# Kernel tuning notes

Measured on AMD Instinct MI355X. Metric: run time of the kernel, lower is better.

The kernel has to match this reference:

```python
import jax, jax.numpy as jnp
import numpy as np

N, H, W = 128, 400, 400          # instances, feature canvas
MS = 28                          # mask_size = pooler_resolution*2
CT, CS = 80, 53                  # thing / stuff classes
STRIDE = 4                       # common_stride
HG, WG = 1600, 1600              # image-resolution gt panoptic
IGNORE = 255
LOSS_W = 1.0


def setup_inputs() -> dict:
    key = jax.random.key(0)
    ks = jax.random.split(key, 8)
    mask_logits = jax.random.normal(ks[0], (N, CT, MS, MS), jnp.float32)
    stuff_logit = jax.random.normal(ks[1], (CS, H, W), jnp.float32)
    thing_logit = jax.random.normal(ks[2], (CT, H, W), jnp.float32)
    # valid boxes in image pixel coords (x0,y0,x2,y2), width/height >= 16 px
    x0 = jax.random.uniform(ks[3], (N,), minval=0.0, maxval=1200.0)
    y0 = jax.random.uniform(ks[4], (N,), minval=0.0, maxval=1200.0)
    wh = jax.random.uniform(ks[5], (N, 2), minval=16.0, maxval=400.0)
    x2 = jnp.minimum(x0 + wh[:, 0], WG - 1.0)
    y2 = jnp.minimum(y0 + wh[:, 1], HG - 1.0)
    bbox = jnp.stack([x0, y0, x2, y2], axis=1).astype(jnp.float32)
    cls_idx = jax.random.randint(ks[6], (N,), 0, CT, dtype=jnp.int32)
    gt_panoptic = jax.random.randint(ks[7], (HG, WG), 0, CS + N, dtype=jnp.int32)
    return {"mask_logits": mask_logits, "stuff_logit": stuff_logit,
            "thing_logit": thing_logit, "bbox": bbox, "cls_idx": cls_idx,
            "gt_panoptic": gt_panoptic}


def _axis_sample(lo, size, grid, src_size):
    """Bilinear sampling coords along one axis (align_corners=False).
    lo: [N] box start (feat px, int); size: [N] box extent; grid: [G].
    Returns (idx0, idx1, frac) each [N, G]."""
    dst = grid[None, :].astype(jnp.float32) - lo[:, None].astype(jnp.float32)
    src = (dst + 0.5) * (src_size / size[:, None].astype(jnp.float32)) - 0.5
    f = jnp.floor(src)
    t = src - f
    i0 = jnp.clip(f, 0, src_size - 1).astype(jnp.int32)
    i1 = jnp.clip(f + 1, 0, src_size - 1).astype(jnp.int32)
    return i0, i1, t


def reference(mask_logits, stuff_logit, thing_logit, bbox, cls_idx, gt_panoptic):
    # _separate_fetch_logits: gather per-instance class channel -> [N, MS, MS]
    ml = mask_logits[jnp.arange(N), cls_idx]

    # _unmap_mask_logit_single: boxes -> feat coords (.long() == floor, boxes >= 0)
    bl = jnp.floor(bbox / STRIDE).astype(jnp.int32)
    x0b, y0b, x2b, y2b = bl[:, 0], bl[:, 1], bl[:, 2], bl[:, 3]
    hh = y2b - y0b + 1
    ww = x2b - x0b + 1
    ys = jnp.arange(H, dtype=jnp.int32)
    xs = jnp.arange(W, dtype=jnp.int32)

    i0, i1, ty = _axis_sample(y0b, hh, ys, MS)   # [N, H]
    j0, j1, tx = _axis_sample(x0b, ww, xs, MS)   # [N, W]

    # separable bilinear: rows [N, H, MS] then cols [N, H, W]
    r0 = jnp.take_along_axis(ml, jnp.broadcast_to(i0[:, :, None], (N, H, MS)), axis=1)
    r1 = jnp.take_along_axis(ml, jnp.broadcast_to(i1[:, :, None], (N, H, MS)), axis=1)
    rows = r0 * (1.0 - ty)[:, :, None] + r1 * ty[:, :, None]
    c0 = jnp.take_along_axis(rows, jnp.broadcast_to(j0[:, None, :], (N, H, W)), axis=2)
    c1 = jnp.take_along_axis(rows, jnp.broadcast_to(j1[:, None, :], (N, H, W)), axis=2)
    val = c0 * (1.0 - tx)[:, None, :] + c1 * tx[:, None, :]

    vy = (ys[None, :] >= jnp.maximum(y0b, 0)[:, None]) & (ys[None, :] <= jnp.minimum(y2b, H - 1)[:, None])
    vx = (xs[None, :] >= jnp.maximum(x0b, 0)[:, None]) & (xs[None, :] <= jnp.minimum(x2b, W - 1)[:, None])
    thing_mask_logit = jnp.where(vy[:, :, None] & vx[:, None, :], val, 0.0)

    # _crop_thing_logit_single: int()/round() based crop window
    bf = bbox / STRIDE
    cx1 = bf[:, 0].astype(jnp.int32)
    cy1 = bf[:, 1].astype(jnp.int32)
    cx2 = (jnp.round(bf[:, 2]) + 1.0).astype(jnp.int32)
    cy2 = (jnp.round(bf[:, 3]) + 1.0).astype(jnp.int32)
    my = (ys[None, :] >= cy1[:, None]) & (ys[None, :] < cy2[:, None])
    mx = (xs[None, :] >= cx1[:, None]) & (xs[None, :] < cx2[:, None])
    thing_sem_logit = jnp.where(my[:, :, None] & mx[:, None, :], thing_logit[cls_idx], 0.0)

    pan_logit = jnp.concatenate(
        [stuff_logit[None], (thing_mask_logit + thing_sem_logit)[None]], axis=1)

    # gt nearest-downsample to feat_size, then CE with ignore_index
    iy = jnp.floor(jnp.arange(H) * (HG / H)).astype(jnp.int32)
    ix = jnp.floor(jnp.arange(W) * (WG / W)).astype(jnp.int32)
    gt_ds = gt_panoptic[iy[:, None], ix[None, :]][None]          # [1, H, W]
    logp = jax.nn.log_softmax(pan_logit, axis=1)
    tgt = jnp.clip(gt_ds, 0, CS + N - 1)
    nll = -jnp.take_along_axis(logp, tgt[:, None], axis=1)[:, 0]  # [1, H, W]
    valid = gt_ds != IGNORE
    pan_loss = LOSS_W * jnp.sum(jnp.where(valid, nll, 0.0)) / jnp.maximum(
        jnp.sum(valid).astype(jnp.float32), 1.0)
    return pan_logit, pan_loss
```

## Files before the change

### kernel.cpp

```cpp
#include <hip/hip_runtime.h>
#include <hip/hip_bf16.h>
#include <math.h>

#define N_   128
#define H_   400
#define W_   400
#define MS_  28
#define CT_  80
#define CS_  53
#define HW_  (H_*W_)
#define NCH_ (CS_ + N_)
#define WG_  1600
#define IGN_ 255

struct NParam {
  int vy_lo, vy_hi, vx_lo, vx_hi;
  int cy1, cy2, cx1, cx2;
  float sy, sx;
  int y0b, x0b;
  int mlbase, thbase;
  int pad0, pad1;
};

__device__ NParam g_par[N_];
__device__ float  g_acc[2];

__global__ void prep_kernel(const float* __restrict__ bbox,
                            const int*   __restrict__ cls_idx) {
  int n = threadIdx.x;
  if (n < 2) g_acc[n] = 0.0f;
  if (n >= N_) return;
  float b0 = bbox[4*n+0]*0.25f, b1 = bbox[4*n+1]*0.25f,
        b2 = bbox[4*n+2]*0.25f, b3 = bbox[4*n+3]*0.25f;
  int x0b = (int)floorf(b0), y0b = (int)floorf(b1);
  int x2b = (int)floorf(b2), y2b = (int)floorf(b3);
  int hh = y2b - y0b + 1, ww = x2b - x0b + 1;
  NParam p;
  p.vy_lo = max(y0b, 0); p.vy_hi = min(y2b, H_-1);
  p.vx_lo = max(x0b, 0); p.vx_hi = min(x2b, W_-1);
  p.cy1 = (int)b1; p.cx1 = (int)b0;
  p.cy2 = (int)(rintf(b3) + 1.0f);
  p.cx2 = (int)(rintf(b2) + 1.0f);
  p.sy = 28.0f / (float)hh; p.sx = 28.0f / (float)ww;
  p.y0b = y0b; p.x0b = x0b;
  int cls = cls_idx[n];
  p.mlbase = (n*CT_ + cls)*(MS_*MS_);
  p.thbase = cls*HW_;
  p.pad0 = 0; p.pad1 = 0;
  g_par[n] = p;
}

__device__ __forceinline__ void lse_update(float v, float& m, float& s) {
  float d = v - m;
  float e = __expf(-fabsf(d));
  s = (d > 0.0f) ? fmaf(s, e, 1.0f) : (s + e);
  m = fmaxf(m, v);
}

__global__ __launch_bounds__(256) void main_kernel(
    const float* __restrict__ mask_logits,
    const float* __restrict__ stuff_logit,
    const float* __restrict__ thing_logit,
    const int*   __restrict__ gt,
    float* __restrict__ out)
{
  int pix = blockIdx.x*256 + threadIdx.x;
  int y = pix / W_;
  int x = pix - y*W_;

  int g = gt[y*(4*WG_) + x*4];
  bool valid = (g != IGN_);
  int tc = min(max(g, 0), NCH_-1);

  float m = -INFINITY, s = 0.0f, vt = 0.0f;

  for (int c = 0; c < CS_; ++c) {
    float v = stuff_logit[c*HW_ + pix];
    out[c*HW_ + pix] = v;
    lse_update(v, m, s);
    if (c == tc) vt = v;
  }

  for (int n = 0; n < N_; ++n) {
    NParam p = g_par[n];
    float v = 0.0f;
    if (y >= p.cy1 && y < p.cy2 && x >= p.cx1 && x < p.cx2)
      v = thing_logit[p.thbase + pix];
    if (y >= p.vy_lo && y <= p.vy_hi && x >= p.vx_lo && x <= p.vx_hi) {
      float srcy = ((float)(y - p.y0b) + 0.5f)*p.sy - 0.5f;
      float fy = floorf(srcy); float ty = srcy - fy;
      int i0 = (int)fminf(fmaxf(fy,        0.0f), (float)(MS_-1));
      int i1 = (int)fminf(fmaxf(fy + 1.0f, 0.0f), (float)(MS_-1));
      float srcx = ((float)(x - p.x0b) + 0.5f)*p.sx - 0.5f;
      float fx = floorf(srcx); float tx = srcx - fx;
      int j0 = (int)fminf(fmaxf(fx,        0.0f), (float)(MS_-1));
      int j1 = (int)fminf(fmaxf(fx + 1.0f, 0.0f), (float)(MS_-1));
      const float* mlp = mask_logits + p.mlbase;
      float a00 = mlp[i0*MS_ + j0], a01 = mlp[i0*MS_ + j1];
      float a10 = mlp[i1*MS_ + j0], a11 = mlp[i1*MS_ + j1];
      float r0 = a00*(1.0f - tx) + a01*tx;
      float r1 = a10*(1.0f - tx) + a11*tx;
      v += r0*(1.0f - ty) + r1*ty;
    }
    int c = CS_ + n;
    out[c*HW_ + pix] = v;
    lse_update(v, m, s);
    if (c == tc) vt = v;
  }

  float nll = valid ? (m + __logf(s) - vt) : 0.0f;
  float cnt = valid ? 1.0f : 0.0f;
  for (int off = 32; off >= 1; off >>= 1) {
    nll += __shfl_down(nll, off, 64);
    cnt += __shfl_down(cnt, off, 64);
  }
  __shared__ float red[8];
  int lane = threadIdx.x & 63, wid = threadIdx.x >> 6;
  if (lane == 0) { red[wid*2] = nll; red[wid*2+1] = cnt; }
  __syncthreads();
  if (threadIdx.x == 0) {
    float ts  = red[0] + red[2] + red[4] + red[6];
    float tcn = red[1] + red[3] + red[5] + red[7];
    atomicAdd(&g_acc[0], ts);
    atomicAdd(&g_acc[1], tcn);
  }
}

__global__ void loss_kernel(float* __restrict__ out) {
  if (threadIdx.x == 0) {
    float loss = g_acc[0] / fmaxf(g_acc[1], 1.0f);
    out[NCH_*HW_] = loss;
  }
}

extern "C" void kernel_launch(void* const* d_in, const int* in_sizes, int n_in,
                              void* d_out, int out_size, void* d_ws, size_t ws_size,
                              hipStream_t stream) {
  const float* mask_logits = (const float*)d_in[0];
  const float* stuff_logit = (const float*)d_in[1];
  const float* thing_logit = (const float*)d_in[2];
  const float* bbox        = (const float*)d_in[3];
  const int*   cls_idx     = (const int*)d_in[4];
  const int*   gt          = (const int*)d_in[5];
  float* out = (float*)d_out;

  prep_kernel<<<1, 128, 0, stream>>>(bbox, cls_idx);
  main_kernel<<<HW_/256, 256, 0, stream>>>(mask_logits, stuff_logit, thing_logit,
                                           gt, out);
  loss_kernel<<<1, 64, 0, stream>>>(out);
}
```

Before: 254.7 us.

## Split channel loop across grid groups with partial log-sum-exp merge

Splits the 181-channel per-pixel loop into 8 channel groups launched as a 2D grid. Each group writes a partial running max and sum to global scratch. A new reduce kernel merges the partials, reads the target logit back from the output, and computes the NLL reduction. This raises parallelism and occupancy in exchange for extra scratch traffic and an additional kernel launch.

```diff
diff --git a/kernel.cpp b/kernel.cpp
--- a/kernel.cpp
+++ b/kernel.cpp
@@ -12,6 +12,8 @@
 #define NCH_ (CS_ + N_)
 #define WG_  1600
 #define IGN_ 255
+#define G_   8
+#define CPG_ 23
 
 struct NParam {
   int vy_lo, vy_hi, vx_lo, vx_hi;
@@ -24,6 +26,8 @@
 
 __device__ NParam g_par[N_];
 __device__ float  g_acc[2];
+__device__ float  g_pm[G_*HW_];
+__device__ float  g_ps[G_*HW_];
 
 __global__ void prep_kernel(const float* __restrict__ bbox,
                             const int*   __restrict__ cls_idx) {
@@ -61,27 +65,25 @@
     const float* __restrict__ mask_logits,
     const float* __restrict__ stuff_logit,
     const float* __restrict__ thing_logit,
-    const int*   __restrict__ gt,
     float* __restrict__ out)
 {
   int pix = blockIdx.x*256 + threadIdx.x;
   int y = pix / W_;
   int x = pix - y*W_;
+  int grp = blockIdx.y;
+  int c0 = grp*CPG_;
+  int c1 = min(NCH_, c0 + CPG_);
 
-  int g = gt[y*(4*WG_) + x*4];
-  bool valid = (g != IGN_);
-  int tc = min(max(g, 0), NCH_-1);
+  float m = -INFINITY, s = 0.0f;
 
-  float m = -INFINITY, s = 0.0f, vt = 0.0f;
-
-  for (int c = 0; c < CS_; ++c) {
+  int c = c0;
+  for (; c < min(c1, CS_); ++c) {
     float v = stuff_logit[c*HW_ + pix];
     out[c*HW_ + pix] = v;
     lse_update(v, m, s);
-    if (c == tc) vt = v;
   }
-
-  for (int n = 0; n < N_; ++n) {
+  for (; c < c1; ++c) {
+    int n = c - CS_;
     NParam p = g_par[n];
     float v = 0.0f;
     if (y >= p.cy1 && y < p.cy2 && x >= p.cx1 && x < p.cx2)
@@ -102,11 +104,37 @@
       float r1 = a10*(1.0f - tx) + a11*tx;
       v += r0*(1.0f - ty) + r1*ty;
     }
-    int c = CS_ + n;
     out[c*HW_ + pix] = v;
     lse_update(v, m, s);
-    if (c == tc) vt = v;
   }
+
+  g_pm[grp*HW_ + pix] = m;
+  g_ps[grp*HW_ + pix] = s;
+}
+
+__global__ __launch_bounds__(256) void reduce_kernel(
+    const int* __restrict__ gt,
+    const float* __restrict__ out_ro,
+    float* __restrict__ dummy)
+{
+  int pix = blockIdx.x*256 + threadIdx.x;
+
+  float m = g_pm[pix], s = g_ps[pix];
+  #pragma unroll
+  for (int g = 1; g < G_; ++g) {
+    float mg = g_pm[g*HW_ + pix];
+    float sg = g_ps[g*HW_ + pix];
+    float M = fmaxf(m, mg);
+    s = s*__expf(m - M) + sg*__expf(mg - M);
+    m = M;
+  }
+
+  int y = pix / W_;
+  int x = pix - y*W_;
+  int g = gt[y*(4*WG_) + x*4];
+  bool valid = (g != IGN_);
+  int tc = min(max(g, 0), NCH_-1);
+  float vt = out_ro[tc*HW_ + pix];
 
   float nll = valid ? (m + __logf(s) - vt) : 0.0f;
   float cnt = valid ? 1.0f : 0.0f;
@@ -124,6 +152,7 @@
     atomicAdd(&g_acc[0], ts);
     atomicAdd(&g_acc[1], tcn);
   }
+  (void)dummy;
 }
 
 __global__ void loss_kernel(float* __restrict__ out) {
@@ -145,7 +174,9 @@
   float* out = (float*)d_out;
 
   prep_kernel<<<1, 128, 0, stream>>>(bbox, cls_idx);
-  main_kernel<<<HW_/256, 256, 0, stream>>>(mask_logits, stuff_logit, thing_logit,
-                                           gt, out);
+  dim3 grid1(HW_/256, G_);
+  main_kernel<<<grid1, 256, 0, stream>>>(mask_logits, stuff_logit, thing_logit,
+                                         out);
+  reduce_kernel<<<HW_/256, 256, 0, stream>>>(gt, out, out);
   loss_kernel<<<1, 64, 0, stream>>>(out);
 }
```

Result: faster. 242.2 us (-4.9%).
